# Optimization experiments

Hardware: AMD Instinct MI355X
Metric: run time of the kernel (lower is better)

The kernel has to match this reference:

```python
import jax, jax.numpy as jnp
import numpy as np

# PiGNNLayer(d_emb=128, n_heads=1, n_neighbors=30); N nodes, E = N*K edges, BSZ graphs
N, K, H, D = 16384, 30, 1, 128
E = N * K
DH = D // H  # d_head
BSZ = 1      # batch_idx is all zeros (see notes: gating broadcast requires bsz==1)


def setup_inputs() -> dict:
    key = jax.random.key(0)
    ks = jax.random.split(key, 16)

    def W(k, i, o):
        return jax.random.normal(k, (i, o), jnp.float32) / np.float32(np.sqrt(i))

    inp = {
        "h": jax.random.normal(ks[0], (N, D), jnp.float32),
        "e": jax.random.normal(ks[1], (E, D), jnp.float32),
        # att_mlp: Linear(3D,D) ReLU Linear(D,D) ReLU Linear(D,H)
        "aw1": W(ks[2], 3 * D, D), "ab1": jnp.zeros((D,), jnp.float32),
        "aw2": W(ks[3], D, D),     "ab2": jnp.zeros((D,), jnp.float32),
        "aw3": W(ks[4], D, H),     "ab3": jnp.zeros((H,), jnp.float32),
        # node_mlp: Linear(2D,D) GELU Linear(D,D) GELU Linear(D,D)
        "nw1": W(ks[5], 2 * D, D), "nb1": jnp.zeros((D,), jnp.float32),
        "nw2": W(ks[6], D, D),     "nb2": jnp.zeros((D,), jnp.float32),
        "nw3": W(ks[7], D, D),     "nb3": jnp.zeros((D,), jnp.float32),
        # to_h: Linear(D, D, bias=False)
        "thw": W(ks[8], H * D, D),
        # gate_mlp: Linear(D,D) ReLU Linear(D,D) ReLU Linear(D,D)
        "gw1": W(ks[9], D, D),  "gb1": jnp.zeros((D,), jnp.float32),
        "gw2": W(ks[10], D, D), "gb2": jnp.zeros((D,), jnp.float32),
        "gw3": W(ks[11], D, D), "gb3": jnp.zeros((D,), jnp.float32),
        # edge_idx[0] = source node i repeated K times (required by '(i j)' reshape)
        "edge_idx": jnp.stack([
            jnp.repeat(jnp.arange(N, dtype=jnp.int32), K),
            jax.random.randint(ks[12], (E,), 0, N, dtype=jnp.int32),
        ]),
        "batch_idx": jnp.zeros((N,), jnp.int32),
    }
    return inp


def reference(h, e, aw1, ab1, aw2, ab2, aw3, ab3,
              nw1, nb1, nw2, nb2, nw3, nb3, thw,
              gw1, gb1, gw2, gb2, gw3, gb3,
              edge_idx, batch_idx):
    src, dst = edge_idx[0], edge_idx[1]
    hi, hj = h[src], h[dst]                       # [E, D] gathers
    cat3 = jnp.concatenate([hi, e, hj], axis=-1)  # [E, 3D]
    cat2 = jnp.concatenate([e, hj], axis=-1)      # [E, 2D]

    # attention logits per head, grouped (i j) -> [H, N, K]
    w = jax.nn.relu(cat3 @ aw1 + ab1)
    w = jax.nn.relu(w @ aw2 + ab2)
    w = (w @ aw3 + ab3)                           # [E, H]
    w = jnp.transpose(w.reshape(N, K, H), (2, 0, 1)) / jnp.sqrt(jnp.float32(DH))
    att = jax.nn.softmax(w, axis=-1)              # softmax over neighbors j

    # values per edge (exact GELU, matching torch nn.GELU default)
    v = jax.nn.gelu(cat2 @ nw1 + nb1, approximate=False)
    v = jax.nn.gelu(v @ nw2 + nb2, approximate=False)
    v = (v @ nw3 + nb3).reshape(N, K, D)          # [N, K, D]

    hh = jnp.einsum('hij,ijd->ihd', att, v).reshape(N, H * D)  # 'h i d -> i (h d)'
    hh = hh @ thw                                 # to_h (no bias)

    # scatter_mean over batch (segment-sum form of the dense-mask trick)
    csum = jax.ops.segment_sum(hh, batch_idx, num_segments=BSZ)
    cnt = jax.ops.segment_sum(jnp.ones((N, 1), hh.dtype), batch_idx, num_segments=BSZ)
    c = csum / cnt                                # [BSZ, D]

    g = jax.nn.relu(c @ gw1 + gb1)
    g = jax.nn.relu(g @ gw2 + gb2)
    g = jax.nn.sigmoid(g @ gw3 + gb3)             # [BSZ, D]
    return hh * g[batch_idx]                      # per-node gate gather
```

## Files before the change

kernel.cpp:

```cpp
#include <hip/hip_runtime.h>
#include <math.h>

#define NN 16384
#define KNB 30
#define NE (NN*KNB)

typedef __attribute__((ext_vector_type(8))) __bf16 bf16x8;
typedef __attribute__((ext_vector_type(4))) float f32x4;
typedef unsigned short ushortT;
typedef __attribute__((ext_vector_type(8))) unsigned short ushort8v;

#define SWZ(r) (((r)&7)<<4)

__device__ __forceinline__ ushortT f2bf(float x){
  __bf16 b = (__bf16)x;
  union { __bf16 b; ushortT u; } v; v.b = b; return v.u;
}
__device__ __forceinline__ float bf2f(ushortT u){
  union { unsigned int u32; float f; } v; v.u32 = ((unsigned int)u) << 16;
  return v.f;
}
__device__ __forceinline__ float bf2f_lo(unsigned int w){
  union { unsigned int u32; float f; } v; v.u32 = w << 16; return v.f;
}
__device__ __forceinline__ float bf2f_hi(unsigned int w){
  union { unsigned int u32; float f; } v; v.u32 = w & 0xffff0000u; return v.f;
}
__device__ __forceinline__ float gelu_f(float x){
  float ax = fabsf(x) * 0.7071067811865476f;
  float t = 1.0f / (1.0f + 0.47047f * ax);
  float poly = t*(0.3480242f + t*(-0.0958798f + t*0.7478556f));
  float er = 1.0f - poly * __expf(-ax*ax);
  er = copysignf(er, x);
  return 0.5f * x * (1.0f + er);
}

__global__ void prep_kernel(const float* __restrict__ h,
                            const float* __restrict__ aw1, const float* __restrict__ nw1,
                            const float* __restrict__ aw2, const float* __restrict__ nw2,
                            const float* __restrict__ nw3, const float* __restrict__ nb3,
                            const float* __restrict__ thw,
                            const float* __restrict__ ab1, const float* __restrict__ nb1,
                            const float* __restrict__ ab2, const float* __restrict__ nb2,
                            ushortT* __restrict__ WF1, ushortT* __restrict__ WF2,
                            float* __restrict__ bias1, float* __restrict__ bias2,
                            float* __restrict__ U, ushortT* __restrict__ WVhP,
                            float* __restrict__ M, float* __restrict__ c3)
{
  __shared__ float sbuf[8*128];
  int tid = threadIdx.x;
  int b = blockIdx.x;

  if (b < 2048) {
    size_t n0 = (size_t)b * 8;
    if (tid < 256) {
      int r = tid >> 5, c = (tid & 31) * 4;
      *(float4*)&sbuf[r*128 + c] = *(const float4*)(h + (n0 + r)*128 + c);
    }
    __syncthreads();
    int d = tid & 127, seg = tid >> 7;
    const float* wbase = (seg == 0) ? (aw1 + d)
                       : (seg == 1) ? (aw1 + 256*128 + d)
                                    : (nw1 + 128*128 + d);
    float s[8] = {0.f,0.f,0.f,0.f,0.f,0.f,0.f,0.f};
    for (int c = 0; c < 128; ++c) {
      float w = wbase[(size_t)c*128];
      #pragma unroll
      for (int r = 0; r < 8; ++r) s[r] += sbuf[r*128 + c] * w;
    }
    if (seg == 0) {
      #pragma unroll
      for (int r = 0; r < 8; ++r) U[(n0 + r)*128 + d] = s[r];
    } else {
      int off = seg - 1;
      #pragma unroll
      for (int r = 0; r < 8; ++r) WVhP[(n0 + r)*256 + 2*d + off] = f2bf(s[r]);
    }
    return;
  }
  if (b < 2107) {
    if (tid >= 256) return;
    int u = (b - 2048) * 256 + tid;
    if (u < 8192) {
      int lane = u & 63, tile = u >> 6;
      int half = tile >> 6, nt = (tile >> 3) & 7, kt = tile & 7;
      int mrow = lane & 15, krow = lane >> 4;
      int n = half*128 + nt*16 + mrow, k0 = kt*32 + krow*8;
      ushort8v o;
      #pragma unroll
      for (int j = 0; j < 8; ++j) {
        int k = k0 + j;
        float v = (half == 0) ? aw1[(128 + k)*128 + n] : nw1[k*128 + (n - 128)];
        o[j] = f2bf(v);
      }
      *(ushort8v*)(WF1 + (size_t)u*8) = o;
      return;
    }
    u -= 8192;
    if (u < 4096) {
      int lane = u & 63, tile = u >> 6;
      int half = tile >> 5, nt = (tile >> 2) & 7, kt = tile & 3;
      int mrow = lane & 15, krow = lane >> 4;
      int n = half*128 + nt*16 + mrow, k0 = kt*32 + krow*8;
      ushort8v o;
      #pragma unroll
      for (int j = 0; j < 8; ++j) {
        int k = k0 + j;
        float v = (half == 0) ? aw2[k*128 + n] : nw2[k*128 + (n - 128)];
        o[j] = f2bf(v);
      }
      *(ushort8v*)(WF2 + (size_t)u*8) = o;
      return;
    }
    u -= 4096;
    if (u < 256) { bias1[u] = (u < 128) ? ab1[u] : nb1[u - 128]; return; }
    u -= 256;
    if (u < 256) { bias2[u] = (u < 128) ? ab2[u] : nb2[u - 128]; return; }
    return;
  }
  {
    if (tid >= 128) return;
    int bb = b - 2107;
    int d = tid;
    sbuf[d] = (bb < 128) ? nw3[bb*128 + d] : nb3[d];
    __syncthreads();
    float s = 0.f;
    for (int n = 0; n < 128; ++n) s += sbuf[n] * thw[n*128 + d];
    if (bb < 128) M[bb*128 + d] = s;
    else c3[d] = s;
  }
}

__global__ __launch_bounds__(512, 8) void edge_kernel(
    const float* __restrict__ e,
    const int* __restrict__ edge_idx,
    const ushortT* __restrict__ WVhP,
    const ushortT* __restrict__ WF1, const ushortT* __restrict__ WF2,
    const float* __restrict__ bias1, const float* __restrict__ bias2,
    const float* __restrict__ aw3, const float* __restrict__ ab3,
    float* __restrict__ hh)
{
  extern __shared__ char smem[];
  char*  Xb   = smem;
  char*  Yb   = smem + 16384;
  float* lgp  = (float*)(smem + 32768);
  float* Ubs  = (float*)(smem + 33792);

  const int tid  = threadIdx.x;
  const int lane = tid & 63;
  const int wid  = tid >> 6;
  const int node = blockIdx.x;
  const long e0 = (long)node * KNB;

  const int mrow = lane & 15, krow = lane >> 4;
  const int ca = wid*16 + mrow;

  float uval = 0.f;
  if (tid < 128) uval = hh[(size_t)node*128 + tid];

  {
    int r = tid >> 4, c8 = tid & 15;
    ushort8v u = {0,0,0,0,0,0,0,0};
    if (r < KNB) {
      const float* src = e + ((size_t)(e0 + r))*128 + c8*8;
      float4 v0 = *(const float4*)src;
      float4 v1 = *(const float4*)(src + 4);
      u[0]=f2bf(v0.x); u[1]=f2bf(v0.y); u[2]=f2bf(v0.z); u[3]=f2bf(v0.w);
      u[4]=f2bf(v1.x); u[5]=f2bf(v1.y); u[6]=f2bf(v1.z); u[7]=f2bf(v1.w);
    }
    *(ushort8v*)(Xb + r*512 + ((c8*16) ^ SWZ(r))) = u;
  }

  unsigned int wv[8];
  #pragma unroll
  for (int g = 0; g < 8; ++g) {
    int row_ = (g >> 2)*16 + krow*4 + (g & 3);
    wv[g] = 0u;
    if (row_ < KNB) {
      int dst = edge_idx[NE + e0 + row_];
      wv[g] = ((const unsigned int*)(WVhP + (size_t)dst*256))[ca];
    }
  }
  if (tid < 128) Ubs[tid] = uval;
  asm volatile("s_waitcnt lgkmcnt(0)" ::: "memory");
  __builtin_amdgcn_s_barrier();

  const float b1a = bias1[ca],       b1n = bias1[128 + ca];
  const float b2a = bias2[ca],       b2n = bias2[128 + ca];
  const float aw3c = aw3[ca] * 0.08838834764831845f;

  f32x4 acc[2][2];
  #pragma unroll
  for (int mt = 0; mt < 2; ++mt)
    #pragma unroll
    for (int j = 0; j < 2; ++j) acc[mt][j] = (f32x4){0.f,0.f,0.f,0.f};

  #pragma unroll
  for (int kt = 0; kt < 4; ++kt) {
    int koff = kt*64 + krow*16;
    bf16x8 a0 = *(const bf16x8*)(Xb + mrow*512 + (koff ^ SWZ(mrow)));
    bf16x8 a1 = *(const bf16x8*)(Xb + (16 + mrow)*512 + (koff ^ SWZ(16 + mrow)));
    bf16x8 ba = *(const bf16x8*)(WF1 + ((size_t)(wid*8 + kt))*512 + lane*8);
    bf16x8 bn = *(const bf16x8*)(WF1 + ((size_t)((8 + wid)*8 + kt))*512 + lane*8);
    acc[0][0] = __builtin_amdgcn_mfma_f32_16x16x32_bf16(a0, ba, acc[0][0], 0, 0, 0);
    acc[1][0] = __builtin_amdgcn_mfma_f32_16x16x32_bf16(a1, ba, acc[1][0], 0, 0, 0);
    acc[0][1] = __builtin_amdgcn_mfma_f32_16x16x32_bf16(a0, bn, acc[0][1], 0, 0, 0);
    acc[1][1] = __builtin_amdgcn_mfma_f32_16x16x32_bf16(a1, bn, acc[1][1], 0, 0, 0);
  }

  {
    const float b1u = b1a + Ubs[ca];
    #pragma unroll
    for (int mt = 0; mt < 2; ++mt)
      #pragma unroll
      for (int rr = 0; rr < 4; ++rr) {
        int row_ = mt*16 + krow*4 + rr;
        int g = mt*4 + rr;
        char* yrow = Yb + row_*512;
        int sw = SWZ(row_);
        float x = fmaxf(acc[mt][0][rr] + b1u + bf2f_lo(wv[g]), 0.f);
        *(ushortT*)(yrow + ((2*ca) ^ sw)) = f2bf(x);
        float y = gelu_f(acc[mt][1][rr] + b1n + bf2f_hi(wv[g]));
        *(ushortT*)(yrow + ((256 + 2*ca) ^ sw)) = f2bf(y);
      }
  }
  __syncthreads();

  #pragma unroll
  for (int mt = 0; mt < 2; ++mt)
    #pragma unroll
    for (int j = 0; j < 2; ++j) acc[mt][j] = (f32x4){0.f,0.f,0.f,0.f};
  #pragma unroll
  for (int kt = 0; kt < 4; ++kt) {
    int koff = kt*64 + krow*16;
    bf16x8 aw0 = *(const bf16x8*)(Yb + mrow*512 + (koff ^ SWZ(mrow)));
    bf16x8 aw1v = *(const bf16x8*)(Yb + (16 + mrow)*512 + (koff ^ SWZ(16 + mrow)));
    bf16x8 av0 = *(const bf16x8*)(Yb + mrow*512 + ((256 + koff) ^ SWZ(mrow)));
    bf16x8 av1 = *(const bf16x8*)(Yb + (16 + mrow)*512 + ((256 + koff) ^ SWZ(16 + mrow)));
    bf16x8 ba = *(const bf16x8*)(WF2 + ((size_t)(wid*4 + kt))*512 + lane*8);
    bf16x8 bn = *(const bf16x8*)(WF2 + ((size_t)((8 + wid)*4 + kt))*512 + lane*8);
    acc[0][0] = __builtin_amdgcn_mfma_f32_16x16x32_bf16(aw0, ba, acc[0][0], 0, 0, 0);
    acc[1][0] = __builtin_amdgcn_mfma_f32_16x16x32_bf16(aw1v, ba, acc[1][0], 0, 0, 0);
    acc[0][1] = __builtin_amdgcn_mfma_f32_16x16x32_bf16(av0, bn, acc[0][1], 0, 0, 0);
    acc[1][1] = __builtin_amdgcn_mfma_f32_16x16x32_bf16(av1, bn, acc[1][1], 0, 0, 0);
  }

  {
    #pragma unroll
    for (int mt = 0; mt < 2; ++mt)
      #pragma unroll
      for (int rr = 0; rr < 4; ++rr) {
        int row_ = mt*16 + krow*4 + rr;
        int sw = SWZ(row_);
        float lsum = fmaxf(acc[mt][0][rr] + b2a, 0.f) * aw3c;
        lsum += __shfl_xor(lsum, 1);
        lsum += __shfl_xor(lsum, 2);
        lsum += __shfl_xor(lsum, 4);
        lsum += __shfl_xor(lsum, 8);
        if (mrow == 0) lgp[wid*32 + row_] = lsum;
        float y = gelu_f(acc[mt][1][rr] + b2n);
        *(ushortT*)(Xb + row_*512 + ((2*ca) ^ sw)) = f2bf(y);
      }
  }
  __syncthreads();

  {
    float x = -INFINITY;
    if (lane < KNB) {
      x = lgp[lane];
      #pragma unroll
      for (int w = 1; w < 8; ++w) x += lgp[w*32 + lane];
    }
    float m = x;
    #pragma unroll
    for (int off = 16; off >= 1; off >>= 1) m = fmaxf(m, __shfl_xor(m, off));
    float p = (lane < KNB) ? __expf(x - m) : 0.f;
    float ssum = p;
    #pragma unroll
    for (int off = 16; off >= 1; off >>= 1) ssum += __shfl_xor(ssum, off);
    float attv = p / ssum;

    int pr = lane & 7, ks = lane >> 3;
    int col0 = wid*16 + pr*2;
    float s0 = 0.f, s1 = 0.f;
    #pragma unroll
    for (int j = 0; j < 4; ++j) {
      int k2 = ks + 8*j;
      float a = __shfl(attv, k2);
      unsigned int w = *(const unsigned int*)(Xb + k2*512 + ((2*col0) ^ SWZ(k2)));
      s0 += a * bf2f_lo(w);
      s1 += a * bf2f_hi(w);
    }
    s0 += __shfl_xor(s0, 8);  s1 += __shfl_xor(s1, 8);
    s0 += __shfl_xor(s0, 16); s1 += __shfl_xor(s1, 16);
    s0 += __shfl_xor(s0, 32); s1 += __shfl_xor(s1, 32);
    if (lane < 8) {
      float2 o; o.x = s0; o.y = s1;
      *(float2*)(hh + (size_t)node*128 + col0) = o;
    }
  }
}

__global__ void reduce1_kernel(const float* __restrict__ hh, float* __restrict__ p2) {
  int b = blockIdx.x, tid = threadIdx.x;
  int d = tid & 127, half = tid >> 7;
  float s = 0.f;
  const float* base = hh + (size_t)(b*64 + half*32)*128 + d;
  #pragma unroll 4
  for (int i = 0; i < 32; ++i) s += base[(size_t)i*128];
  __shared__ float ps[256];
  ps[tid] = s; __syncthreads();
  if (tid < 128) p2[b*128 + tid] = ps[tid] + ps[tid + 128];
}

__global__ void gate_kernel(const float* __restrict__ p2,
                            const float* __restrict__ M, const float* __restrict__ c3,
                            const float* __restrict__ gw1, const float* __restrict__ gb1,
                            const float* __restrict__ gw2, const float* __restrict__ gb2,
                            const float* __restrict__ gw3, const float* __restrict__ gb3,
                            float* __restrict__ gout) {
  int tid = threadIdx.x;
  int d = tid & 127, half = tid >> 7;
  float s = 0.f;
  for (int i = 0; i < 128; ++i) s += p2[(half*128 + i)*128 + d];
  __shared__ float ps[256];
  __shared__ float cv[128], cv2[128], y1[128], y2[128];
  ps[tid] = s; __syncthreads();
  if (tid < 128) cv[tid] = (ps[tid] + ps[tid+128]) * (1.f / (float)NN);
  __syncthreads();
  if (tid < 128) {
    float a = c3[tid];
    for (int c = 0; c < 128; ++c) a += cv[c] * M[c*128 + tid];
    cv2[tid] = a;
  }
  __syncthreads();
  if (tid < 128) {
    float a = gb1[tid];
    for (int c = 0; c < 128; ++c) a += cv2[c] * gw1[c*128 + tid];
    y1[tid] = fmaxf(a, 0.f);
  }
  __syncthreads();
  if (tid < 128) {
    float a = gb2[tid];
    for (int c = 0; c < 128; ++c) a += y1[c] * gw2[c*128 + tid];
    y2[tid] = fmaxf(a, 0.f);
  }
  __syncthreads();
  if (tid < 128) {
    float a = gb3[tid];
    for (int c = 0; c < 128; ++c) a += y2[c] * gw3[c*128 + tid];
    gout[tid] = 1.f / (1.f + __expf(-a));
  }
}

__global__ void toh_scale_kernel(float* __restrict__ hh, const float* __restrict__ M,
                                 const float* __restrict__ c3,
                                 const float* __restrict__ gv)
{
  __shared__ float hs[16][128];
  int tid = threadIdx.x;
  size_t n0 = (size_t)blockIdx.x * 16;
  {
    int r = tid >> 4, c = (tid & 15) * 8;
    const float* src = hh + (n0 + r)*128 + c;
    *(float4*)&hs[r][c]     = *(const float4*)src;
    *(float4*)&hs[r][c + 4] = *(const float4*)(src + 4);
  }
  __syncthreads();
  int d = tid & 127, gq = tid >> 7;
  float s[8] = {0.f,0.f,0.f,0.f,0.f,0.f,0.f,0.f};
  for (int c = 0; c < 128; ++c) {
    float w = M[c*128 + d];
    #pragma unroll
    for (int r = 0; r < 8; ++r) s[r] += hs[gq*8 + r][c] * w;
  }
  float gd = gv[d];
  float cd = c3[d];
  #pragma unroll
  for (int r = 0; r < 8; ++r) hh[(n0 + gq*8 + r)*128 + d] = (s[r] + cd) * gd;
}

extern "C" void kernel_launch(void* const* d_in, const int* in_sizes, int n_in,
                              void* d_out, int out_size, void* d_ws, size_t ws_size,
                              hipStream_t stream) {
  const float* h   = (const float*)d_in[0];
  const float* e   = (const float*)d_in[1];
  const float* aw1 = (const float*)d_in[2];
  const float* ab1 = (const float*)d_in[3];
  const float* aw2 = (const float*)d_in[4];
  const float* ab2 = (const float*)d_in[5];
  const float* aw3 = (const float*)d_in[6];
  const float* ab3 = (const float*)d_in[7];
  const float* nw1 = (const float*)d_in[8];
  const float* nb1 = (const float*)d_in[9];
  const float* nw2 = (const float*)d_in[10];
  const float* nb2 = (const float*)d_in[11];
  const float* nw3 = (const float*)d_in[12];
  const float* nb3 = (const float*)d_in[13];
  const float* thw = (const float*)d_in[14];
  const float* gw1 = (const float*)d_in[15];
  const float* gb1 = (const float*)d_in[16];
  const float* gw2 = (const float*)d_in[17];
  const float* gb2 = (const float*)d_in[18];
  const float* gw3 = (const float*)d_in[19];
  const float* gb3 = (const float*)d_in[20];
  const int* edge_idx = (const int*)d_in[21];

  char* ws = (char*)d_ws;
  ushortT* WF1 = (ushortT*)(ws + 0);
  ushortT* WF2 = (ushortT*)(ws + 131072);
  float* bias1 = (float*)(ws + 196608);
  float* bias2 = (float*)(ws + 197632);
  float* p2    = (float*)(ws + 198656);
  float* gout  = (float*)(ws + 329728);
  float* Mw    = (float*)(ws + 330240);
  float* c3w   = (float*)(ws + 395776);
  ushortT* WVhP= (ushortT*)(ws + 396288);
  float* hh    = (float*)d_out;

  prep_kernel<<<2236, 384, 0, stream>>>(h, aw1, nw1, aw2, nw2, nw3, nb3, thw,
                                        ab1, nb1, ab2, nb2,
                                        WF1, WF2, bias1, bias2,
                                        hh, WVhP, Mw, c3w);

  const int SMEM = 34304;
  hipFuncSetAttribute((const void*)edge_kernel,
                      hipFuncAttributeMaxDynamicSharedMemorySize, SMEM);
  edge_kernel<<<NN, 512, SMEM, stream>>>(e, edge_idx, WVhP, WF1, WF2,
                                         bias1, bias2, aw3, ab3, hh);

  reduce1_kernel<<<256, 256, 0, stream>>>(hh, p2);
  gate_kernel<<<1, 256, 0, stream>>>(p2, Mw, c3w, gw1, gb1, gw2, gb2, gw3, gb3, gout);
  toh_scale_kernel<<<NN/16, 256, 0, stream>>>(hh, Mw, c3w, gout);
}
```

Measured before the change: 306.3 us.

## Process eight nodes per edge-kernel block with double-buffered prefetch of next edge rows

The edge kernel becomes persistent over 8 nodes per block instead of one, with grid reduced to NN/8. It ping-pongs the X/Y shared buffers and prefetches the next node's e rows into registers during the second MLP layer, then writes them to shared memory after the barrier. The aim is to amortise block launch and bias loads and hide global load latency, at the cost of fewer blocks (2048), more barriers per node and extra register pressure.

After: 1.011 ms. 3.3x slower.

```diff
diff --git a/kernel.cpp b/kernel.cpp
--- a/kernel.cpp
+++ b/kernel.cpp
@@ -141,163 +141,179 @@
     float* __restrict__ hh)
 {
   extern __shared__ char smem[];
-  char*  Xb   = smem;
-  char*  Yb   = smem + 16384;
-  float* lgp  = (float*)(smem + 32768);
-  float* Ubs  = (float*)(smem + 33792);
+  float* lgp = (float*)(smem + 32768);
 
   const int tid  = threadIdx.x;
   const int lane = tid & 63;
   const int wid  = tid >> 6;
-  const int node = blockIdx.x;
-  const long e0 = (long)node * KNB;
-
   const int mrow = lane & 15, krow = lane >> 4;
   const int ca = wid*16 + mrow;
-
-  float uval = 0.f;
-  if (tid < 128) uval = hh[(size_t)node*128 + tid];
+  const int sr = tid >> 4, sc8 = tid & 15;
+  const int n0 = blockIdx.x * 8;
+
+  const float b1a = bias1[ca],       b1n = bias1[128 + ca];
+  const float b2a = bias2[ca],       b2n = bias2[128 + ca];
+  const float aw3c = aw3[ca] * 0.08838834764831845f;
 
   {
-    int r = tid >> 4, c8 = tid & 15;
     ushort8v u = {0,0,0,0,0,0,0,0};
-    if (r < KNB) {
-      const float* src = e + ((size_t)(e0 + r))*128 + c8*8;
+    if (sr < KNB) {
+      const float* src = e + ((size_t)n0*KNB + sr)*128 + sc8*8;
       float4 v0 = *(const float4*)src;
       float4 v1 = *(const float4*)(src + 4);
       u[0]=f2bf(v0.x); u[1]=f2bf(v0.y); u[2]=f2bf(v0.z); u[3]=f2bf(v0.w);
       u[4]=f2bf(v1.x); u[5]=f2bf(v1.y); u[6]=f2bf(v1.z); u[7]=f2bf(v1.w);
     }
-    *(ushort8v*)(Xb + r*512 + ((c8*16) ^ SWZ(r))) = u;
-  }
-
-  unsigned int wv[8];
-  #pragma unroll
-  for (int g = 0; g < 8; ++g) {
-    int row_ = (g >> 2)*16 + krow*4 + (g & 3);
-    wv[g] = 0u;
-    if (row_ < KNB) {
-      int dst = edge_idx[NE + e0 + row_];
-      wv[g] = ((const unsigned int*)(WVhP + (size_t)dst*256))[ca];
-    }
-  }
-  if (tid < 128) Ubs[tid] = uval;
-  asm volatile("s_waitcnt lgkmcnt(0)" ::: "memory");
-  __builtin_amdgcn_s_barrier();
-
-  const float b1a = bias1[ca],       b1n = bias1[128 + ca];
-  const float b2a = bias2[ca],       b2n = bias2[128 + ca];
-  const float aw3c = aw3[ca] * 0.08838834764831845f;
-
-  f32x4 acc[2][2];
-  #pragma unroll
-  for (int mt = 0; mt < 2; ++mt)
-    #pragma unroll
-    for (int j = 0; j < 2; ++j) acc[mt][j] = (f32x4){0.f,0.f,0.f,0.f};
-
-  #pragma unroll
-  for (int kt = 0; kt < 4; ++kt) {
-    int koff = kt*64 + krow*16;
-    bf16x8 a0 = *(const bf16x8*)(Xb + mrow*512 + (koff ^ SWZ(mrow)));
-    bf16x8 a1 = *(const bf16x8*)(Xb + (16 + mrow)*512 + (koff ^ SWZ(16 + mrow)));
-    bf16x8 ba = *(const bf16x8*)(WF1 + ((size_t)(wid*8 + kt))*512 + lane*8);
-    bf16x8 bn = *(const bf16x8*)(WF1 + ((size_t)((8 + wid)*8 + kt))*512 + lane*8);
-    acc[0][0] = __builtin_amdgcn_mfma_f32_16x16x32_bf16(a0, ba, acc[0][0], 0, 0, 0);
-    acc[1][0] = __builtin_amdgcn_mfma_f32_16x16x32_bf16(a1, ba, acc[1][0], 0, 0, 0);
-    acc[0][1] = __builtin_amdgcn_mfma_f32_16x16x32_bf16(a0, bn, acc[0][1], 0, 0, 0);
-    acc[1][1] = __builtin_amdgcn_mfma_f32_16x16x32_bf16(a1, bn, acc[1][1], 0, 0, 0);
-  }
-
-  {
-    const float b1u = b1a + Ubs[ca];
+    *(ushort8v*)(smem + sr*512 + ((sc8*16) ^ SWZ(sr))) = u;
+  }
+  __syncthreads();
+
+  for (int it = 0; it < 8; ++it) {
+    const int node = n0 + it;
+    const long e0 = (long)node * KNB;
+    char* Xc = smem + ((it & 1) ? 16384 : 0);
+    char* Yc = smem + ((it & 1) ? 0 : 16384);
+
+    float uu = hh[(size_t)node*128 + ca];
+    unsigned int wv[8];
+    #pragma unroll
+    for (int g = 0; g < 8; ++g) {
+      int row_ = (g >> 2)*16 + krow*4 + (g & 3);
+      wv[g] = 0u;
+      if (row_ < KNB) {
+        int dst = edge_idx[NE + e0 + row_];
+        wv[g] = ((const unsigned int*)(WVhP + (size_t)dst*256))[ca];
+      }
+    }
+
+    f32x4 acc[2][2];
     #pragma unroll
     for (int mt = 0; mt < 2; ++mt)
       #pragma unroll
-      for (int rr = 0; rr < 4; ++rr) {
-        int row_ = mt*16 + krow*4 + rr;
-        int g = mt*4 + rr;
-        char* yrow = Yb + row_*512;
-        int sw = SWZ(row_);
-        float x = fmaxf(acc[mt][0][rr] + b1u + bf2f_lo(wv[g]), 0.f);
-        *(ushortT*)(yrow + ((2*ca) ^ sw)) = f2bf(x);
-        float y = gelu_f(acc[mt][1][rr] + b1n + bf2f_hi(wv[g]));
-        *(ushortT*)(yrow + ((256 + 2*ca) ^ sw)) = f2bf(y);
-      }
-  }
-  __syncthreads();
-
-  #pragma unroll
-  for (int mt = 0; mt < 2; ++mt)
-    #pragma unroll
-    for (int j = 0; j < 2; ++j) acc[mt][j] = (f32x4){0.f,0.f,0.f,0.f};
-  #pragma unroll
-  for (int kt = 0; kt < 4; ++kt) {
-    int koff = kt*64 + krow*16;
-    bf16x8 aw0 = *(const bf16x8*)(Yb + mrow*512 + (koff ^ SWZ(mrow)));
-    bf16x8 aw1v = *(const bf16x8*)(Yb + (16 + mrow)*512 + (koff ^ SWZ(16 + mrow)));
-    bf16x8 av0 = *(const bf16x8*)(Yb + mrow*512 + ((256 + koff) ^ SWZ(mrow)));
-    bf16x8 av1 = *(const bf16x8*)(Yb + (16 + mrow)*512 + ((256 + koff) ^ SWZ(16 + mrow)));
-    bf16x8 ba = *(const bf16x8*)(WF2 + ((size_t)(wid*4 + kt))*512 + lane*8);
-    bf16x8 bn = *(const bf16x8*)(WF2 + ((size_t)((8 + wid)*4 + kt))*512 + lane*8);
-    acc[0][0] = __builtin_amdgcn_mfma_f32_16x16x32_bf16(aw0, ba, acc[0][0], 0, 0, 0);
-    acc[1][0] = __builtin_amdgcn_mfma_f32_16x16x32_bf16(aw1v, ba, acc[1][0], 0, 0, 0);
-    acc[0][1] = __builtin_amdgcn_mfma_f32_16x16x32_bf16(av0, bn, acc[0][1], 0, 0, 0);
-    acc[1][1] = __builtin_amdgcn_mfma_f32_16x16x32_bf16(av1, bn, acc[1][1], 0, 0, 0);
-  }
-
-  {
+      for (int j = 0; j < 2; ++j) acc[mt][j] = (f32x4){0.f,0.f,0.f,0.f};
+
+    #pragma unroll
+    for (int kt = 0; kt < 4; ++kt) {
+      int koff = kt*64 + krow*16;
+      bf16x8 a0 = *(const bf16x8*)(Xc + mrow*512 + (koff ^ SWZ(mrow)));
+      bf16x8 a1 = *(const bf16x8*)(Xc + (16 + mrow)*512 + (koff ^ SWZ(16 + mrow)));
+      bf16x8 ba = *(const bf16x8*)(WF1 + ((size_t)(wid*8 + kt))*512 + lane*8);
+      bf16x8 bn = *(const bf16x8*)(WF1 + ((size_t)((8 + wid)*8 + kt))*512 + lane*8);
+      acc[0][0] = __builtin_amdgcn_mfma_f32_16x16x32_bf16(a0, ba, acc[0][0], 0, 0, 0);
+      acc[1][0] = __builtin_amdgcn_mfma_f32_16x16x32_bf16(a1, ba, acc[1][0], 0, 0, 0);
+      acc[0][1] = __builtin_amdgcn_mfma_f32_16x16x32_bf16(a0, bn, acc[0][1], 0, 0, 0);
+      acc[1][1] = __builtin_amdgcn_mfma_f32_16x16x32_bf16(a1, bn, acc[1][1], 0, 0, 0);
+    }
+
+    {
+      const float b1u = b1a + uu;
+      #pragma unroll
+      for (int mt = 0; mt < 2; ++mt)
+        #pragma unroll
+        for (int rr = 0; rr < 4; ++rr) {
+          int row_ = mt*16 + krow*4 + rr;
+          int g = mt*4 + rr;
+          char* yrow = Yc + row_*512;
+          int sw = SWZ(row_);
+          float x = fmaxf(acc[mt][0][rr] + b1u + bf2f_lo(wv[g]), 0.f);
+          *(ushortT*)(yrow + ((2*ca) ^ sw)) = f2bf(x);
+          float y = gelu_f(acc[mt][1][rr] + b1n + bf2f_hi(wv[g]));
+          *(ushortT*)(yrow + ((256 + 2*ca) ^ sw)) = f2bf(y);
+        }
+    }
+    __syncthreads();
+
+    float enx[8];
+    if (it < 7 && sr < KNB) {
+      const float* src = e + ((size_t)(node + 1)*KNB + sr)*128 + sc8*8;
+      float4 v0 = *(const float4*)src;
+      float4 v1 = *(const float4*)(src + 4);
+      enx[0]=v0.x; enx[1]=v0.y; enx[2]=v0.z; enx[3]=v0.w;
+      enx[4]=v1.x; enx[5]=v1.y; enx[6]=v1.z; enx[7]=v1.w;
+    }
+
     #pragma unroll
     for (int mt = 0; mt < 2; ++mt)
       #pragma unroll
-      for (int rr = 0; rr < 4; ++rr) {
-        int row_ = mt*16 + krow*4 + rr;
-        int sw = SWZ(row_);
-        float lsum = fmaxf(acc[mt][0][rr] + b2a, 0.f) * aw3c;
-        lsum += __shfl_xor(lsum, 1);
-        lsum += __shfl_xor(lsum, 2);
-        lsum += __shfl_xor(lsum, 4);
-        lsum += __shfl_xor(lsum, 8);
-        if (mrow == 0) lgp[wid*32 + row_] = lsum;
-        float y = gelu_f(acc[mt][1][rr] + b2n);
-        *(ushortT*)(Xb + row_*512 + ((2*ca) ^ sw)) = f2bf(y);
-      }
-  }
-  __syncthreads();
-
-  {
-    float x = -INFINITY;
-    if (lane < KNB) {
-      x = lgp[lane];
-      #pragma unroll
-      for (int w = 1; w < 8; ++w) x += lgp[w*32 + lane];
-    }
-    float m = x;
-    #pragma unroll
-    for (int off = 16; off >= 1; off >>= 1) m = fmaxf(m, __shfl_xor(m, off));
-    float p = (lane < KNB) ? __expf(x - m) : 0.f;
-    float ssum = p;
-    #pragma unroll
-    for (int off = 16; off >= 1; off >>= 1) ssum += __shfl_xor(ssum, off);
-    float attv = p / ssum;
-
-    int pr = lane & 7, ks = lane >> 3;
-    int col0 = wid*16 + pr*2;
-    float s0 = 0.f, s1 = 0.f;
-    #pragma unroll
-    for (int j = 0; j < 4; ++j) {
-      int k2 = ks + 8*j;
-      float a = __shfl(attv, k2);
-      unsigned int w = *(const unsigned int*)(Xb + k2*512 + ((2*col0) ^ SWZ(k2)));
-      s0 += a * bf2f_lo(w);
-      s1 += a * bf2f_hi(w);
-    }
-    s0 += __shfl_xor(s0, 8);  s1 += __shfl_xor(s1, 8);
-    s0 += __shfl_xor(s0, 16); s1 += __shfl_xor(s1, 16);
-    s0 += __shfl_xor(s0, 32); s1 += __shfl_xor(s1, 32);
-    if (lane < 8) {
-      float2 o; o.x = s0; o.y = s1;
-      *(float2*)(hh + (size_t)node*128 + col0) = o;
-    }
+      for (int j = 0; j < 2; ++j) acc[mt][j] = (f32x4){0.f,0.f,0.f,0.f};
+    #pragma unroll
+    for (int kt = 0; kt < 4; ++kt) {
+      int koff = kt*64 + krow*16;
+      bf16x8 aw0 = *(const bf16x8*)(Yc + mrow*512 + (koff ^ SWZ(mrow)));
+      bf16x8 aw1v = *(const bf16x8*)(Yc + (16 + mrow)*512 + (koff ^ SWZ(16 + mrow)));
+      bf16x8 av0 = *(const bf16x8*)(Yc + mrow*512 + ((256 + koff) ^ SWZ(mrow)));
+      bf16x8 av1 = *(const bf16x8*)(Yc + (16 + mrow)*512 + ((256 + koff) ^ SWZ(16 + mrow)));
+      bf16x8 ba = *(const bf16x8*)(WF2 + ((size_t)(wid*4 + kt))*512 + lane*8);
+      bf16x8 bn = *(const bf16x8*)(WF2 + ((size_t)((8 + wid)*4 + kt))*512 + lane*8);
+      acc[0][0] = __builtin_amdgcn_mfma_f32_16x16x32_bf16(aw0, ba, acc[0][0], 0, 0, 0);
+      acc[1][0] = __builtin_amdgcn_mfma_f32_16x16x32_bf16(aw1v, ba, acc[1][0], 0, 0, 0);
+      acc[0][1] = __builtin_amdgcn_mfma_f32_16x16x32_bf16(av0, bn, acc[0][1], 0, 0, 0);
+      acc[1][1] = __builtin_amdgcn_mfma_f32_16x16x32_bf16(av1, bn, acc[1][1], 0, 0, 0);
+    }
+
+    {
+      #pragma unroll
+      for (int mt = 0; mt < 2; ++mt)
+        #pragma unroll
+        for (int rr = 0; rr < 4; ++rr) {
+          int row_ = mt*16 + krow*4 + rr;
+          int sw = SWZ(row_);
+          float lsum = fmaxf(acc[mt][0][rr] + b2a, 0.f) * aw3c;
+          lsum += __shfl_xor(lsum, 1);
+          lsum += __shfl_xor(lsum, 2);
+          lsum += __shfl_xor(lsum, 4);
+          lsum += __shfl_xor(lsum, 8);
+          if (mrow == 0) lgp[wid*32 + row_] = lsum;
+          float y = gelu_f(acc[mt][1][rr] + b2n);
+          *(ushortT*)(Xc + row_*512 + ((2*ca) ^ sw)) = f2bf(y);
+        }
+    }
+    __syncthreads();
+
+    if (it < 7) {
+      ushort8v u = {0,0,0,0,0,0,0,0};
+      if (sr < KNB) {
+        u[0]=f2bf(enx[0]); u[1]=f2bf(enx[1]); u[2]=f2bf(enx[2]); u[3]=f2bf(enx[3]);
+        u[4]=f2bf(enx[4]); u[5]=f2bf(enx[5]); u[6]=f2bf(enx[6]); u[7]=f2bf(enx[7]);
+      }
+      *(ushort8v*)(Yc + sr*512 + ((sc8*16) ^ SWZ(sr))) = u;
+    }
+    {
+      float x = -INFINITY;
+      if (lane < KNB) {
+        x = lgp[lane];
+        #pragma unroll
+        for (int w = 1; w < 8; ++w) x += lgp[w*32 + lane];
+      }
+      float m = x;
+      #pragma unroll
+      for (int off = 16; off >= 1; off >>= 1) m = fmaxf(m, __shfl_xor(m, off));
+      float p = (lane < KNB) ? __expf(x - m) : 0.f;
+      float ssum = p;
+      #pragma unroll
+      for (int off = 16; off >= 1; off >>= 1) ssum += __shfl_xor(ssum, off);
+      float attv = p / ssum;
+
+      int pr = lane & 7, ks = lane >> 3;
+      int col0 = wid*16 + pr*2;
+      float s0 = 0.f, s1 = 0.f;
+      #pragma unroll
+      for (int j = 0; j < 4; ++j) {
+        int k2 = ks + 8*j;
+        float a = __shfl(attv, k2);
+        unsigned int w = *(const unsigned int*)(Xc + k2*512 + ((2*col0) ^ SWZ(k2)));
+        s0 += a * bf2f_lo(w);
+        s1 += a * bf2f_hi(w);
+      }
+      s0 += __shfl_xor(s0, 8);  s1 += __shfl_xor(s1, 8);
+      s0 += __shfl_xor(s0, 16); s1 += __shfl_xor(s1, 16);
+      s0 += __shfl_xor(s0, 32); s1 += __shfl_xor(s1, 32);
+      if (lane < 8) {
+        float2 o; o.x = s0; o.y = s1;
+        *(float2*)(hh + (size_t)node*128 + col0) = o;
+      }
+    }
+    __syncthreads();
   }
 }
 
@@ -423,11 +439,11 @@
                                         WF1, WF2, bias1, bias2,
                                         hh, WVhP, Mw, c3w);
 
-  const int SMEM = 34304;
+  const int SMEM = 33792;
   hipFuncSetAttribute((const void*)edge_kernel,
                       hipFuncAttributeMaxDynamicSharedMemorySize, SMEM);
-  edge_kernel<<<NN, 512, SMEM, stream>>>(e, edge_idx, WVhP, WF1, WF2,
-                                         bias1, bias2, aw3, ab3, hh);
+  edge_kernel<<<NN/8, 512, SMEM, stream>>>(e, edge_idx, WVhP, WF1, WF2,
+                                           bias1, bias2, aw3, ab3, hh);
 
   reduce1_kernel<<<256, 256, 0, stream>>>(hh, p2);
   gate_kernel<<<1, 256, 0, stream>>>(p2, Mw, c3w, gw1, gb1, gw2, gb2, gw3, gb3, gout);
```

## Split node projection out of prep into a bf16 MFMA kernel

Applied to the files above, without the earlier changes.

Moves the per-node projections of h (U, and the packed Wh/Vh values) out of the scalar FMA loop in the prep kernel into a dedicated kernel that uses bf16 MFMA, with the weights pre-packed into fragment layout by the pack kernel. The prep kernel becomes a small weight-packing kernel. This targets the cost of the scalar per-node GEMM, in exchange for an extra launch and bf16 rounding of h and U, which were previously computed in fp32.

Result: faster. 279.9 us (-8.6%).

```diff
diff --git a/kernel.cpp b/kernel.cpp
--- a/kernel.cpp
+++ b/kernel.cpp
@@ -35,52 +35,23 @@
   return 0.5f * x * (1.0f + er);
 }
 
-__global__ void prep_kernel(const float* __restrict__ h,
-                            const float* __restrict__ aw1, const float* __restrict__ nw1,
+__global__ void pack_kernel(const float* __restrict__ aw1, const float* __restrict__ nw1,
                             const float* __restrict__ aw2, const float* __restrict__ nw2,
                             const float* __restrict__ nw3, const float* __restrict__ nb3,
                             const float* __restrict__ thw,
                             const float* __restrict__ ab1, const float* __restrict__ nb1,
                             const float* __restrict__ ab2, const float* __restrict__ nb2,
                             ushortT* __restrict__ WF1, ushortT* __restrict__ WF2,
+                            ushortT* __restrict__ WB,
                             float* __restrict__ bias1, float* __restrict__ bias2,
-                            float* __restrict__ U, ushortT* __restrict__ WVhP,
                             float* __restrict__ M, float* __restrict__ c3)
 {
-  __shared__ float sbuf[8*128];
+  __shared__ float sbuf[128];
   int tid = threadIdx.x;
   int b = blockIdx.x;
 
-  if (b < 2048) {
-    size_t n0 = (size_t)b * 8;
-    if (tid < 256) {
-      int r = tid >> 5, c = (tid & 31) * 4;
-      *(float4*)&sbuf[r*128 + c] = *(const float4*)(h + (n0 + r)*128 + c);
-    }
-    __syncthreads();
-    int d = tid & 127, seg = tid >> 7;
-    const float* wbase = (seg == 0) ? (aw1 + d)
-                       : (seg == 1) ? (aw1 + 256*128 + d)
-                                    : (nw1 + 128*128 + d);
-    float s[8] = {0.f,0.f,0.f,0.f,0.f,0.f,0.f,0.f};
-    for (int c = 0; c < 128; ++c) {
-      float w = wbase[(size_t)c*128];
-      #pragma unroll
-      for (int r = 0; r < 8; ++r) s[r] += sbuf[r*128 + c] * w;
-    }
-    if (seg == 0) {
-      #pragma unroll
-      for (int r = 0; r < 8; ++r) U[(n0 + r)*128 + d] = s[r];
-    } else {
-      int off = seg - 1;
-      #pragma unroll
-      for (int r = 0; r < 8; ++r) WVhP[(n0 + r)*256 + 2*d + off] = f2bf(s[r]);
-    }
-    return;
-  }
-  if (b < 2107) {
-    if (tid >= 256) return;
-    int u = (b - 2048) * 256 + tid;
+  if (b < 74) {
+    int u = b * 256 + tid;
     if (u < 8192) {
       int lane = u & 63, tile = u >> 6;
       int half = tile >> 6, nt = (tile >> 3) & 7, kt = tile & 7;
@@ -113,6 +84,24 @@
       return;
     }
     u -= 4096;
+    if (u < 6144) {
+      int lane = u & 63, tile = u >> 6;
+      int tt = tile >> 2, kt = tile & 3;
+      int mrow = lane & 15, krow = lane >> 4;
+      int n = (tt & 7)*16 + mrow, k0 = kt*32 + krow*8;
+      ushort8v o;
+      #pragma unroll
+      for (int j = 0; j < 8; ++j) {
+        int k = k0 + j;
+        float v = (tt < 8)  ? aw1[k*128 + n]
+                : (tt < 16) ? aw1[(256 + k)*128 + n]
+                            : nw1[(128 + k)*128 + n];
+        o[j] = f2bf(v);
+      }
+      *(ushort8v*)(WB + (size_t)u*8) = o;
+      return;
+    }
+    u -= 6144;
     if (u < 256) { bias1[u] = (u < 128) ? ab1[u] : nb1[u - 128]; return; }
     u -= 256;
     if (u < 256) { bias2[u] = (u < 128) ? ab2[u] : nb2[u - 128]; return; }
@@ -120,7 +109,7 @@
   }
   {
     if (tid >= 128) return;
-    int bb = b - 2107;
+    int bb = b - 74;
     int d = tid;
     sbuf[d] = (bb < 128) ? nw3[bb*128 + d] : nb3[d];
     __syncthreads();
@@ -128,6 +117,70 @@
     for (int n = 0; n < 128; ++n) s += sbuf[n] * thw[n*128 + d];
     if (bb < 128) M[bb*128 + d] = s;
     else c3[d] = s;
+  }
+}
+
+__global__ __launch_bounds__(512, 8) void uwvh_kernel(
+    const float* __restrict__ h, const ushortT* __restrict__ WB,
+    float* __restrict__ U, ushortT* __restrict__ WVhP)
+{
+  __shared__ char Ah[8192];
+
+  const int tid  = threadIdx.x;
+  const int lane = tid & 63;
+  const int wid  = tid >> 6;
+  const int mrow = lane & 15, krow = lane >> 4;
+  const size_t n0 = (size_t)blockIdx.x * 32;
+
+  {
+    int r = tid >> 4, c8 = tid & 15;
+    const float* src = h + (n0 + r)*128 + c8*8;
+    float4 v0 = *(const float4*)src;
+    float4 v1 = *(const float4*)(src + 4);
+    ushort8v u;
+    u[0]=f2bf(v0.x); u[1]=f2bf(v0.y); u[2]=f2bf(v0.z); u[3]=f2bf(v0.w);
+    u[4]=f2bf(v1.x); u[5]=f2bf(v1.y); u[6]=f2bf(v1.z); u[7]=f2bf(v1.w);
+    *(ushort8v*)(Ah + r*256 + ((c8*16) ^ SWZ(r))) = u;
+  }
+  __syncthreads();
+
+  f32x4 acc[2][3];
+  #pragma unroll
+  for (int mt = 0; mt < 2; ++mt)
+    #pragma unroll
+    for (int j = 0; j < 3; ++j) acc[mt][j] = (f32x4){0.f,0.f,0.f,0.f};
+
+  #pragma unroll
+  for (int kt = 0; kt < 4; ++kt) {
+    int koff = kt*64 + krow*16;
+    bf16x8 a0 = *(const bf16x8*)(Ah + mrow*256 + (koff ^ SWZ(mrow)));
+    bf16x8 a1 = *(const bf16x8*)(Ah + (16 + mrow)*256 + (koff ^ SWZ(16 + mrow)));
+    #pragma unroll
+    for (int j = 0; j < 3; ++j) {
+      bf16x8 bfr = *(const bf16x8*)(WB + ((size_t)((wid*3 + j)*4 + kt))*512 + lane*8);
+      acc[0][j] = __builtin_amdgcn_mfma_f32_16x16x32_bf16(a0, bfr, acc[0][j], 0, 0, 0);
+      acc[1][j] = __builtin_amdgcn_mfma_f32_16x16x32_bf16(a1, bfr, acc[1][j], 0, 0, 0);
+    }
+  }
+
+  #pragma unroll
+  for (int j = 0; j < 3; ++j) {
+    int t = wid*3 + j;
+    #pragma unroll
+    for (int mt = 0; mt < 2; ++mt)
+      #pragma unroll
+      for (int rr = 0; rr < 4; ++rr) {
+        int row = mt*16 + krow*4 + rr;
+        size_t node = n0 + row;
+        float v = acc[mt][j][rr];
+        if (t < 8) {
+          U[node*128 + t*16 + mrow] = v;
+        } else if (t < 16) {
+          WVhP[node*256 + 2*((t - 8)*16 + mrow)] = f2bf(v);
+        } else {
+          WVhP[node*256 + 2*((t - 16)*16 + mrow) + 1] = f2bf(v);
+        }
+      }
   }
 }
 
@@ -416,12 +469,14 @@
   float* Mw    = (float*)(ws + 330240);
   float* c3w   = (float*)(ws + 395776);
   ushortT* WVhP= (ushortT*)(ws + 396288);
+  ushortT* WB  = (ushortT*)(ws + 8784896);
   float* hh    = (float*)d_out;
 
-  prep_kernel<<<2236, 384, 0, stream>>>(h, aw1, nw1, aw2, nw2, nw3, nb3, thw,
-                                        ab1, nb1, ab2, nb2,
-                                        WF1, WF2, bias1, bias2,
-                                        hh, WVhP, Mw, c3w);
+  pack_kernel<<<203, 256, 0, stream>>>(aw1, nw1, aw2, nw2, nw3, nb3, thw,
+                                       ab1, nb1, ab2, nb2,
+                                       WF1, WF2, WB, bias1, bias2, Mw, c3w);
+
+  uwvh_kernel<<<NN/32, 512, 0, stream>>>(h, WB, hh, WVhP);
 
   const int SMEM = 34304;
   hipFuncSetAttribute((const void*)edge_kernel,
```
